# Kernel optimization log

Hardware: AMD Instinct MI355X
Metric: run time of the kernel (lower is better)

## Reference

```python
import jax, jax.numpy as jnp
import numpy as np

DIM_Q = 512
DIM_K = 512
DIM_V = 512
NUM_HEADS = 8
B, NQ, NK = 8, 1024, 1024
EPS = 1e-5


def _layer_norm(x, gamma, beta):
    mu = jnp.mean(x, axis=-1, keepdims=True)
    var = jnp.var(x, axis=-1, keepdims=True)
    return (x - mu) * jax.lax.rsqrt(var + EPS) * gamma + beta


def setup_inputs() -> dict:
    key = jax.random.key(0)
    ks = jax.random.split(key, 12)

    def lin(k, fan_in, fan_out):
        bound = 1.0 / np.sqrt(fan_in)
        kw, kb = jax.random.split(k)
        W = jax.random.uniform(kw, (fan_in, fan_out), jnp.float32, -bound, bound)
        b = jax.random.uniform(kb, (fan_out,), jnp.float32, -bound, bound)
        return W, b

    Q = jax.random.normal(ks[0], (B, NQ, DIM_Q), jnp.float32)
    K = jax.random.normal(ks[1], (B, NK, DIM_K), jnp.float32)
    Wq, bq = lin(ks[2], DIM_Q, DIM_V)
    Wk, bk = lin(ks[3], DIM_K, DIM_V)
    Wv, bv = lin(ks[4], DIM_K, DIM_V)
    Wo, bo = lin(ks[5], DIM_V, DIM_V)
    g0 = jnp.ones((DIM_V,), jnp.float32)
    be0 = jnp.zeros((DIM_V,), jnp.float32)
    g1 = jnp.ones((DIM_V,), jnp.float32)
    be1 = jnp.zeros((DIM_V,), jnp.float32)
    return {"Q": Q, "K": K, "Wq": Wq, "bq": bq, "Wk": Wk, "bk": bk,
            "Wv": Wv, "bv": bv, "Wo": Wo, "bo": bo,
            "g0": g0, "be0": be0, "g1": g1, "be1": be1}


def reference(Q, K, Wq, bq, Wk, bk, Wv, bv, Wo, bo, g0, be0, g1, be1):
    H = NUM_HEADS
    d = DIM_V // H
    b, nq, _ = Q.shape
    nk = K.shape[1]

    Qp = (Q @ Wq + bq).reshape(b, nq, H, d)   # [B,Nq,H,d]
    Kp = (K @ Wk + bk).reshape(b, nk, H, d)   # [B,Nk,H,d]
    Vp = (K @ Wv + bv).reshape(b, nk, H, d)   # [B,Nk,H,d]

    # NOTE: original scales by sqrt(dim_V), not sqrt(head_dim)
    scores = jnp.einsum("bqhd,bkhd->bhqk", Qp, Kp) / jnp.sqrt(
        jnp.asarray(DIM_V, Qp.dtype))
    A = jax.nn.softmax(scores, axis=-1)                     # [B,H,Nq,Nk]
    O = Qp + jnp.einsum("bhqk,bkhd->bqhd", A, Vp)           # residual inside heads
    O = O.reshape(b, nq, DIM_V)
    O = _layer_norm(O, g0, be0)
    O = O + jax.nn.relu(O @ Wo + bo)
    O = _layer_norm(O, g1, be1)
    return O
```

## Files before the change

kernel.cpp:

```cpp
#include <hip/hip_runtime.h>
#include <hip/hip_bf16.h>

typedef __attribute__((ext_vector_type(8))) short short8;
typedef __attribute__((ext_vector_type(4))) short s16x4;
typedef __attribute__((ext_vector_type(4))) float f32x4;

#define DIMV 512
#define NHEAD 8
#define NBATCH 8
#define NQL 1024
#define NKL 1024
#define QSCALE (0.04419417382415922f * 1.44269504088896340f)

__device__ __forceinline__ short f2bf(float f) {
    unsigned int u = __float_as_uint(f);
    unsigned int r = (u + 0x7fffu + ((u >> 16) & 1u)) >> 16;
    return (short)r;
}
__device__ __forceinline__ float bf2f(short s) {
    return __uint_as_float(((unsigned int)(unsigned short)s) << 16);
}
__device__ __forceinline__ unsigned cvt_pk_bf16(float a, float b) {
    unsigned r;
    asm("v_cvt_pk_bf16_f32 %0, %1, %2" : "=v"(r) : "v"(a), "v"(b));
    return r;
}
__device__ __forceinline__ short8 pack8(float4 x, float4 y) {
    union { unsigned u[4]; short8 s; } u;
    u.u[0] = cvt_pk_bf16(x.x, x.y); u.u[1] = cvt_pk_bf16(x.z, x.w);
    u.u[2] = cvt_pk_bf16(y.x, y.y); u.u[3] = cvt_pk_bf16(y.z, y.w);
    return u.s;
}

__global__ void k_transpose_w4(const float* __restrict__ w0, const float* __restrict__ w1,
                               const float* __restrict__ w2, const float* __restrict__ w3,
                               short* __restrict__ t0, short* __restrict__ t1,
                               short* __restrict__ t2, short* __restrict__ t3) {
    __shared__ float tile[32][33];
    const float* W; short* Wt;
    int z = blockIdx.z;
    if (z == 0)      { W = w0; Wt = t0; }
    else if (z == 1) { W = w1; Wt = t1; }
    else if (z == 2) { W = w2; Wt = t2; }
    else             { W = w3; Wt = t3; }
    int tx = threadIdx.x, ty = threadIdx.y;
    int n0 = blockIdx.x * 32, k0 = blockIdx.y * 32;
    #pragma unroll
    for (int r = 0; r < 4; ++r)
        tile[ty + r * 8][tx] = W[(size_t)(k0 + ty + r * 8) * DIMV + n0 + tx];
    __syncthreads();
    #pragma unroll
    for (int r = 0; r < 4; ++r)
        Wt[(size_t)(n0 + ty + r * 8) * DIMV + k0 + tx] = f2bf(tile[tx][ty + r * 8]);
}

__global__ __launch_bounds__(256) void k_transpose_v(const short* __restrict__ KVp,
                                                     short* __restrict__ VT) {
    __shared__ short tile[64][72];
    int tid = threadIdx.x;
    int bid = blockIdx.x;
    int kt = bid & 15, h = (bid >> 4) & 7, b = bid >> 7;
    const short* src = KVp + ((size_t)(b * 1024 + kt * 64)) * 1024 + 512 + h * 64;
    short* dst = VT + ((size_t)(b * 512 + h * 64)) * 1024 + kt * 64;
    #pragma unroll
    for (int p = 0; p < 2; ++p) {
        int idx = p * 256 + tid;
        int r = idx >> 3, dc = (idx & 7) * 8;
        short8 v = *reinterpret_cast<const short8*>(&src[(size_t)r * 1024 + dc]);
        #pragma unroll
        for (int j = 0; j < 8; ++j) tile[dc + j][r] = v[j];
    }
    __syncthreads();
    #pragma unroll
    for (int p = 0; p < 2; ++p) {
        int idx = p * 256 + tid;
        int r = idx >> 3, kc = (idx & 7) * 8;
        *reinterpret_cast<short8*>(&dst[(size_t)r * 1024 + kc]) =
            *reinterpret_cast<const short8*>(&tile[r][kc]);
    }
}

#define GLS 72
template<int MODE, bool AF32, int NBX, int LDC>
__global__ __launch_bounds__(256) void k_gemm(
    const void* __restrict__ Av, const short* __restrict__ Bt,
    const float* __restrict__ bias, const float* __restrict__ bias2,
    short* __restrict__ outB, const short* __restrict__ residB)
{
    __shared__ __align__(16) short As[64 * GLS];
    __shared__ __align__(16) short Bs[64 * GLS];
    int tid = threadIdx.x;
    int lane = tid & 63, wid = tid >> 6;
    int wr = wid >> 1, wc = wid & 1;
    int c = lane & 15, g = lane >> 4;
    int bid = blockIdx.x;
    int xcd = bid & 7, slot = bid >> 3;
    int bx = slot % NBX;
    int by = xcd + 8 * (slot / NBX);
    int m0 = by * 64, n0 = bx * 64;

    int r0 = tid >> 3, kc = (tid & 7) * 8;
    const short* Bg = Bt + (size_t)(n0 + r0) * 512 + kc;

    f32x4 acc[2][2] = {};
    short8 b0 = *reinterpret_cast<const short8*>(Bg);
    short8 b1 = *reinterpret_cast<const short8*>(Bg + 32 * 512);

    if (AF32) {
        const float* Ag = (const float*)Av + (size_t)(m0 + r0) * 512 + kc;
        float4 a00 = *reinterpret_cast<const float4*>(Ag);
        float4 a01 = *reinterpret_cast<const float4*>(Ag + 4);
        float4 a10 = *reinterpret_cast<const float4*>(Ag + 32 * 512);
        float4 a11 = *reinterpret_cast<const float4*>(Ag + 32 * 512 + 4);

        for (int k0 = 0; k0 < 512; k0 += 64) {
            *reinterpret_cast<short8*>(&As[r0 * GLS + kc]) = pack8(a00, a01);
            *reinterpret_cast<short8*>(&As[(r0 + 32) * GLS + kc]) = pack8(a10, a11);
            *reinterpret_cast<short8*>(&Bs[r0 * GLS + kc]) = b0;
            *reinterpret_cast<short8*>(&Bs[(r0 + 32) * GLS + kc]) = b1;
            __syncthreads();
            if (k0 < 448) {
                a00 = *reinterpret_cast<const float4*>(Ag + k0 + 64);
                a01 = *reinterpret_cast<const float4*>(Ag + k0 + 64 + 4);
                a10 = *reinterpret_cast<const float4*>(Ag + k0 + 64 + 32 * 512);
                a11 = *reinterpret_cast<const float4*>(Ag + k0 + 64 + 32 * 512 + 4);
                b0 = *reinterpret_cast<const short8*>(Bg + k0 + 64);
                b1 = *reinterpret_cast<const short8*>(Bg + k0 + 64 + 32 * 512);
            }
            #pragma unroll
            for (int ks = 0; ks < 2; ++ks) {
                short8 af[2], bfr[2];
                #pragma unroll
                for (int i = 0; i < 2; ++i)
                    af[i] = *reinterpret_cast<short8*>(&As[(wr * 32 + i * 16 + c) * GLS + ks * 32 + g * 8]);
                #pragma unroll
                for (int j = 0; j < 2; ++j)
                    bfr[j] = *reinterpret_cast<short8*>(&Bs[(wc * 32 + j * 16 + c) * GLS + ks * 32 + g * 8]);
                #pragma unroll
                for (int i = 0; i < 2; ++i)
                    #pragma unroll
                    for (int j = 0; j < 2; ++j)
                        acc[i][j] = __builtin_amdgcn_mfma_f32_16x16x32_bf16(af[i], bfr[j], acc[i][j], 0, 0, 0);
            }
            __syncthreads();
        }
    } else {
        const short* Ag = (const short*)Av + (size_t)(m0 + r0) * 512 + kc;
        short8 a0 = *reinterpret_cast<const short8*>(Ag);
        short8 a1 = *reinterpret_cast<const short8*>(Ag + 32 * 512);

        for (int k0 = 0; k0 < 512; k0 += 64) {
            *reinterpret_cast<short8*>(&As[r0 * GLS + kc]) = a0;
            *reinterpret_cast<short8*>(&As[(r0 + 32) * GLS + kc]) = a1;
            *reinterpret_cast<short8*>(&Bs[r0 * GLS + kc]) = b0;
            *reinterpret_cast<short8*>(&Bs[(r0 + 32) * GLS + kc]) = b1;
            __syncthreads();
            if (k0 < 448) {
                a0 = *reinterpret_cast<const short8*>(Ag + k0 + 64);
                a1 = *reinterpret_cast<const short8*>(Ag + k0 + 64 + 32 * 512);
                b0 = *reinterpret_cast<const short8*>(Bg + k0 + 64);
                b1 = *reinterpret_cast<const short8*>(Bg + k0 + 64 + 32 * 512);
            }
            #pragma unroll
            for (int ks = 0; ks < 2; ++ks) {
                short8 af[2], bfr[2];
                #pragma unroll
                for (int i = 0; i < 2; ++i)
                    af[i] = *reinterpret_cast<short8*>(&As[(wr * 32 + i * 16 + c) * GLS + ks * 32 + g * 8]);
                #pragma unroll
                for (int j = 0; j < 2; ++j)
                    bfr[j] = *reinterpret_cast<short8*>(&Bs[(wc * 32 + j * 16 + c) * GLS + ks * 32 + g * 8]);
                #pragma unroll
                for (int i = 0; i < 2; ++i)
                    #pragma unroll
                    for (int j = 0; j < 2; ++j)
                        acc[i][j] = __builtin_amdgcn_mfma_f32_16x16x32_bf16(af[i], bfr[j], acc[i][j], 0, 0, 0);
            }
            __syncthreads();
        }
    }

    #pragma unroll
    for (int i = 0; i < 2; ++i)
        #pragma unroll
        for (int j = 0; j < 2; ++j) {
            int row = m0 + wr * 32 + i * 16 + g * 4;
            int col = n0 + wc * 32 + j * 16 + c;
            float bb = (MODE == 1 && n0 >= 512) ? bias2[col - 512] : bias[col];
            #pragma unroll
            for (int q = 0; q < 4; ++q) {
                size_t idx = (size_t)(row + q) * LDC + col;
                float v = acc[i][j][q] + bb;
                if (MODE == 0)      outB[idx] = f2bf(v * QSCALE);
                else if (MODE == 1) outB[idx] = f2bf(v);
                else {
                    size_t ridx = (size_t)(row + q) * 512 + col;
                    outB[idx] = f2bf(bf2f(residB[ridx]) + fmaxf(v, 0.f));
                }
            }
        }
}

__global__ __launch_bounds__(256) void k_attn(
    const short* __restrict__ Qb, const short* __restrict__ Kb,
    const short* __restrict__ VTb, const short* __restrict__ RgBase,
    short* __restrict__ Out)
{
    constexpr float RSCALE = 1.0f / QSCALE;
    __shared__ __align__(16) short Ks[64 * 72];
    __shared__ __align__(16) short Vt[64 * 72];
    __shared__ __align__(16) short Ps[64 * 72];
    int tid = threadIdx.x;
    int lane = tid & 63, w = tid >> 6;
    int c = lane & 15, g = lane >> 4;
    int bid = blockIdx.x;
    int xcd = bid & 7, slot = bid >> 3;
    int qb = slot & 15;
    int grp = xcd + 8 * (slot >> 4);
    int h = grp & 7, b = grp >> 3;
    const short* Qg = Qb + (size_t)(b * NQL + qb * 64) * 512 + h * 64;
    const short* Kg = Kb + (size_t)b * NKL * 1024 + h * 64;
    const short* VTg = VTb + (size_t)(b * 512 + h * 64) * NKL;
    const short* Rg = RgBase + (size_t)(b * NQL + qb * 64) * 512 + h * 64;
    short* Og = Out + (size_t)(b * NQL + qb * 64) * 512 + h * 64;

    short8 qf[2];
    #pragma unroll
    for (int ks = 0; ks < 2; ++ks)
        qf[ks] = *reinterpret_cast<const short8*>(&Qg[(size_t)(w * 16 + c) * 512 + ks * 32 + g * 8]);

    int kr[2], kd[2];
    #pragma unroll
    for (int p = 0; p < 2; ++p) {
        int idx = p * 256 + tid;
        kr[p] = idx >> 3; kd[p] = (idx & 7) * 8;
    }

    short8 kreg[2], vreg[2];
    #pragma unroll
    for (int p = 0; p < 2; ++p) {
        kreg[p] = *reinterpret_cast<const short8*>(&Kg[(size_t)kr[p] * 1024 + kd[p]]);
        vreg[p] = *reinterpret_cast<const short8*>(&VTg[(size_t)kr[p] * 1024 + kd[p]]);
    }
    #pragma unroll
    for (int p = 0; p < 2; ++p) {
        *reinterpret_cast<short8*>(&Ks[kr[p] * 72 + kd[p]]) = kreg[p];
        *reinterpret_cast<short8*>(&Vt[kr[p] * 72 + kd[p]]) = vreg[p];
    }
    __syncthreads();

    float m = -1e30f, l = 0.f;
    f32x4 o[4] = {};

    for (int t = 0; t < 16; ++t) {
        if (t < 15) {
            const short* Kn = Kg + (size_t)(t + 1) * 64 * 1024;
            const short* Vn = VTg + (size_t)(t + 1) * 64;
            #pragma unroll
            for (int p = 0; p < 2; ++p) {
                kreg[p] = *reinterpret_cast<const short8*>(&Kn[(size_t)kr[p] * 1024 + kd[p]]);
                vreg[p] = *reinterpret_cast<const short8*>(&Vn[(size_t)kr[p] * 1024 + kd[p]]);
            }
        }

        f32x4 s[4] = {};
        #pragma unroll
        for (int ks = 0; ks < 2; ++ks) {
            #pragma unroll
            for (int i = 0; i < 4; ++i) {
                short8 ak = *reinterpret_cast<short8*>(&Ks[(i * 16 + c) * 72 + ks * 32 + g * 8]);
                s[i] = __builtin_amdgcn_mfma_f32_16x16x32_bf16(ak, qf[ks], s[i], 0, 0, 0);
            }
        }

        float r0 = fmaxf(fmaxf(s[0][0], s[0][1]), fmaxf(s[0][2], s[0][3]));
        float r1 = fmaxf(fmaxf(s[1][0], s[1][1]), fmaxf(s[1][2], s[1][3]));
        float r2 = fmaxf(fmaxf(s[2][0], s[2][1]), fmaxf(s[2][2], s[2][3]));
        float r3 = fmaxf(fmaxf(s[3][0], s[3][1]), fmaxf(s[3][2], s[3][3]));
        float rowm = fmaxf(fmaxf(r0, r1), fmaxf(r2, r3));
        rowm = fmaxf(rowm, __shfl_xor(rowm, 16));
        rowm = fmaxf(rowm, __shfl_xor(rowm, 32));
        if (!__all(rowm <= m + 8.f)) {
            float mnew = fmaxf(m, rowm);
            float corr = __builtin_amdgcn_exp2f(m - mnew);
            l *= corr;
            float cq[4];
            #pragma unroll
            for (int q = 0; q < 4; ++q) cq[q] = __shfl(corr, g * 4 + q);
            #pragma unroll
            for (int jf = 0; jf < 4; ++jf)
                #pragma unroll
                for (int q = 0; q < 4; ++q)
                    o[jf][q] *= cq[q];
            m = mnew;
        }
        float psum = 0.f;
        #pragma unroll
        for (int i = 0; i < 4; ++i) {
            float p0 = __builtin_amdgcn_exp2f(s[i][0] - m);
            float p1 = __builtin_amdgcn_exp2f(s[i][1] - m);
            float p2 = __builtin_amdgcn_exp2f(s[i][2] - m);
            float p3 = __builtin_amdgcn_exp2f(s[i][3] - m);
            psum += (p0 + p1) + (p2 + p3);
            uint2 pw;
            pw.x = cvt_pk_bf16(p0, p1);
            pw.y = cvt_pk_bf16(p2, p3);
            *reinterpret_cast<uint2*>(&Ps[(w * 16 + c) * 72 + i * 16 + g * 4]) = pw;
        }
        psum += __shfl_xor(psum, 16);
        psum += __shfl_xor(psum, 32);
        l += psum;

        #pragma unroll
        for (int ks = 0; ks < 2; ++ks) {
            short8 pa = *reinterpret_cast<short8*>(&Ps[(w * 16 + c) * 72 + ks * 32 + g * 8]);
            #pragma unroll
            for (int jf = 0; jf < 4; ++jf) {
                short8 vb = *reinterpret_cast<short8*>(&Vt[(jf * 16 + c) * 72 + ks * 32 + g * 8]);
                o[jf] = __builtin_amdgcn_mfma_f32_16x16x32_bf16(pa, vb, o[jf], 0, 0, 0);
            }
        }

        if (t < 15) {
            __syncthreads();
            #pragma unroll
            for (int p = 0; p < 2; ++p) {
                *reinterpret_cast<short8*>(&Ks[kr[p] * 72 + kd[p]]) = kreg[p];
                *reinterpret_cast<short8*>(&Vt[kr[p] * 72 + kd[p]]) = vreg[p];
            }
            __syncthreads();
        }
    }

    float linv = 1.f / l;
    float lq[4];
    #pragma unroll
    for (int q = 0; q < 4; ++q) lq[q] = __shfl(linv, g * 4 + q);
    #pragma unroll
    for (int jf = 0; jf < 4; ++jf)
        #pragma unroll
        for (int q = 0; q < 4; ++q) {
            int r = w * 16 + g * 4 + q;
            int d = jf * 16 + c;
            size_t idx = (size_t)r * 512 + d;
            Og[idx] = f2bf(o[jf][q] * lq[q] + bf2f(Rg[idx]) * RSCALE);
        }
}

__global__ __launch_bounds__(64) void k_ln(
    const short* __restrict__ inB,
    float* __restrict__ outF, short* __restrict__ outB,
    const float* __restrict__ gamma, const float* __restrict__ beta)
{
    int row = blockIdx.x, lane = threadIdx.x;
    float vals[8];
    short8 v = *reinterpret_cast<const short8*>(&inB[(size_t)row * 512 + lane * 8]);
    #pragma unroll
    for (int j = 0; j < 8; ++j) vals[j] = bf2f(v[j]);
    float sum = 0.f, sq = 0.f;
    #pragma unroll
    for (int j = 0; j < 8; ++j) { sum += vals[j]; sq += vals[j] * vals[j]; }
    #pragma unroll
    for (int mask = 32; mask; mask >>= 1) {
        sum += __shfl_xor(sum, mask);
        sq  += __shfl_xor(sq, mask);
    }
    float mean = sum * (1.f / 512.f);
    float var  = sq * (1.f / 512.f) - mean * mean;
    float rstd = rsqrtf(var + 1e-5f);
    float y[8];
    #pragma unroll
    for (int j = 0; j < 8; ++j) {
        int col = lane * 8 + j;
        y[j] = (vals[j] - mean) * rstd * gamma[col] + beta[col];
    }
    size_t base = (size_t)row * 512 + lane * 8;
    if (outF) {
        float4 o0 = {y[0], y[1], y[2], y[3]};
        float4 o1 = {y[4], y[5], y[6], y[7]};
        *reinterpret_cast<float4*>(&outF[base]) = o0;
        *reinterpret_cast<float4*>(&outF[base + 4]) = o1;
    }
    if (outB) {
        int4 p;
        p.x = cvt_pk_bf16(y[0], y[1]); p.y = cvt_pk_bf16(y[2], y[3]);
        p.z = cvt_pk_bf16(y[4], y[5]); p.w = cvt_pk_bf16(y[6], y[7]);
        *reinterpret_cast<int4*>(&outB[base]) = p;
    }
}

extern "C" void kernel_launch(void* const* d_in, const int* in_sizes, int n_in,
                              void* d_out, int out_size, void* d_ws, size_t ws_size,
                              hipStream_t stream) {
    const float* Q   = (const float*)d_in[0];
    const float* K   = (const float*)d_in[1];
    const float* Wq  = (const float*)d_in[2];
    const float* bq  = (const float*)d_in[3];
    const float* Wk  = (const float*)d_in[4];
    const float* bk  = (const float*)d_in[5];
    const float* Wv  = (const float*)d_in[6];
    const float* bv  = (const float*)d_in[7];
    const float* Wo  = (const float*)d_in[8];
    const float* bo  = (const float*)d_in[9];
    const float* g0  = (const float*)d_in[10];
    const float* be0 = (const float*)d_in[11];
    const float* g1  = (const float*)d_in[12];
    const float* be1 = (const float*)d_in[13];
    float* out = (float*)d_out;
    char* ws = (char*)d_ws;
    const size_t MB = 1024 * 1024;

    short* Oa    = (short*)(ws + 0);
    short* Wqt   = (short*)(ws + 16 * MB);
    short* Wkvt  = (short*)(ws + 16 * MB + 512 * 1024);
    short* Wot   = (short*)(ws + 17 * MB + 512 * 1024);
    short* VT    = (short*)(ws + 18 * MB);
    short* Qpb   = (short*)(ws + 34 * MB);
    short* KVp   = (short*)(ws + 42 * MB);
    short* ln0b  = (short*)(ws + 34 * MB);
    short* out2b = (short*)(ws + 42 * MB);

    dim3 tb(32, 8), tg(16, 16, 4);
    k_transpose_w4<<<tg, tb, 0, stream>>>(Wq, Wk, Wv, Wo,
                                          Wqt, Wkvt, Wkvt + 512 * 512, Wot);

    k_gemm<0, true, 8, 512><<<1024, 256, 0, stream>>>(Q, Wqt, bq, nullptr, Qpb, nullptr);
    k_gemm<1, true, 16, 1024><<<2048, 256, 0, stream>>>(K, Wkvt, bk, bv, KVp, nullptr);

    k_transpose_v<<<NBATCH * NHEAD * 16, 256, 0, stream>>>(KVp, VT);

    k_attn<<<NBATCH * NHEAD * (NQL / 64), 256, 0, stream>>>(Qpb, KVp, VT, Qpb, Oa);

    k_ln<<<NBATCH * NQL, 64, 0, stream>>>(Oa, nullptr, ln0b, g0, be0);
    k_gemm<2, false, 8, 512><<<1024, 256, 0, stream>>>(ln0b, Wot, bo, nullptr, out2b, ln0b);
    k_ln<<<NBATCH * NQL, 64, 0, stream>>>(out2b, out, nullptr, g1, be1);
}
```

Measured before the change: 110.1 us.

## Double-buffer attention K/V tiles via direct global-to-LDS loads with swizzle

The attention kernel now stages K and V^T tiles with global_load_lds straight into double-buffered, XOR-swizzled shared memory, replacing register staging and two barriers per iteration with one. Blocks grow to 512 threads covering 128 query rows, so each K/V tile is reused by twice as many waves. The aim is to overlap tile loads with MFMA work, cut LDS bank conflicts and halve K/V traffic per query. In exchange, LDS use per block rises, fewer blocks run (512), the XCD-aware block mapping is dropped, and the code relies on the async LDS load finishing before the single barrier.

```diff
diff --git a/kernel.cpp b/kernel.cpp
--- a/kernel.cpp
+++ b/kernel.cpp
@@ -30,6 +30,11 @@
     u.u[0] = cvt_pk_bf16(x.x, x.y); u.u[1] = cvt_pk_bf16(x.z, x.w);
     u.u[2] = cvt_pk_bf16(y.x, y.y); u.u[3] = cvt_pk_bf16(y.z, y.w);
     return u.s;
+}
+__device__ __forceinline__ void gload16(const void* g, void* l) {
+    __builtin_amdgcn_global_load_lds(
+        (const __attribute__((address_space(1))) unsigned int*)g,
+        (__attribute__((address_space(3))) unsigned int*)l, 16, 0, 0);
 }
 
 __global__ void k_transpose_w4(const float* __restrict__ w0, const float* __restrict__ w1,
@@ -201,66 +206,54 @@
         }
 }
 
-__global__ __launch_bounds__(256) void k_attn(
+__global__ __launch_bounds__(512) void k_attn(
     const short* __restrict__ Qb, const short* __restrict__ Kb,
     const short* __restrict__ VTb, const short* __restrict__ RgBase,
     short* __restrict__ Out)
 {
     constexpr float RSCALE = 1.0f / QSCALE;
-    __shared__ __align__(16) short Ks[64 * 72];
-    __shared__ __align__(16) short Vt[64 * 72];
-    __shared__ __align__(16) short Ps[64 * 72];
+    __shared__ __align__(16) short Ks[2][64 * 64];
+    __shared__ __align__(16) short Vt[2][64 * 64];
+    __shared__ __align__(16) short Ps[128 * 72];
     int tid = threadIdx.x;
     int lane = tid & 63, w = tid >> 6;
     int c = lane & 15, g = lane >> 4;
     int bid = blockIdx.x;
-    int xcd = bid & 7, slot = bid >> 3;
-    int qb = slot & 15;
-    int grp = xcd + 8 * (slot >> 4);
+    int grp = bid & 63, qb = bid >> 6;
     int h = grp & 7, b = grp >> 3;
-    const short* Qg = Qb + (size_t)(b * NQL + qb * 64) * 512 + h * 64;
+    const short* Qg = Qb + (size_t)(b * NQL + qb * 128) * 512 + h * 64;
     const short* Kg = Kb + (size_t)b * NKL * 1024 + h * 64;
     const short* VTg = VTb + (size_t)(b * 512 + h * 64) * NKL;
-    const short* Rg = RgBase + (size_t)(b * NQL + qb * 64) * 512 + h * 64;
-    short* Og = Out + (size_t)(b * NQL + qb * 64) * 512 + h * 64;
+    const short* Rg = RgBase + (size_t)(b * NQL + qb * 128) * 512 + h * 64;
+    short* Og = Out + (size_t)(b * NQL + qb * 128) * 512 + h * 64;
 
     short8 qf[2];
     #pragma unroll
     for (int ks = 0; ks < 2; ++ks)
         qf[ks] = *reinterpret_cast<const short8*>(&Qg[(size_t)(w * 16 + c) * 512 + ks * 32 + g * 8]);
 
-    int kr[2], kd[2];
-    #pragma unroll
-    for (int p = 0; p < 2; ++p) {
-        int idx = p * 256 + tid;
-        kr[p] = idx >> 3; kd[p] = (idx & 7) * 8;
-    }
-
-    short8 kreg[2], vreg[2];
-    #pragma unroll
-    for (int p = 0; p < 2; ++p) {
-        kreg[p] = *reinterpret_cast<const short8*>(&Kg[(size_t)kr[p] * 1024 + kd[p]]);
-        vreg[p] = *reinterpret_cast<const short8*>(&VTg[(size_t)kr[p] * 1024 + kd[p]]);
-    }
-    #pragma unroll
-    for (int p = 0; p < 2; ++p) {
-        *reinterpret_cast<short8*>(&Ks[kr[p] * 72 + kd[p]]) = kreg[p];
-        *reinterpret_cast<short8*>(&Vt[kr[p] * 72 + kd[p]]) = vreg[p];
-    }
+    int sr = tid >> 3, ss = tid & 7;
+    int sg = ss ^ (sr & 7);
+    const short* Kgc = Kg + (size_t)sr * 1024 + sg * 8;
+    const short* Vgc = VTg + (size_t)sr * 1024 + sg * 8;
+    char* KsB = (char*)&Ks[0][0];
+    char* VtB = (char*)&Vt[0][0];
+    int wbase = (tid & ~63) * 16;
+
+    gload16(Kgc, KsB + wbase);
+    gload16(Vgc, VtB + wbase);
     __syncthreads();
 
     float m = -1e30f, l = 0.f;
     f32x4 o[4] = {};
+    int swz = (c & 7) * 8;
 
     for (int t = 0; t < 16; ++t) {
+        int cur = t & 1;
         if (t < 15) {
-            const short* Kn = Kg + (size_t)(t + 1) * 64 * 1024;
-            const short* Vn = VTg + (size_t)(t + 1) * 64;
-            #pragma unroll
-            for (int p = 0; p < 2; ++p) {
-                kreg[p] = *reinterpret_cast<const short8*>(&Kn[(size_t)kr[p] * 1024 + kd[p]]);
-                vreg[p] = *reinterpret_cast<const short8*>(&Vn[(size_t)kr[p] * 1024 + kd[p]]);
-            }
+            int nxt = cur ^ 1;
+            gload16(Kgc + (size_t)(t + 1) * 64 * 1024, KsB + nxt * 8192 + wbase);
+            gload16(Vgc + (t + 1) * 64, VtB + nxt * 8192 + wbase);
         }
 
         f32x4 s[4] = {};
@@ -268,7 +261,8 @@
         for (int ks = 0; ks < 2; ++ks) {
             #pragma unroll
             for (int i = 0; i < 4; ++i) {
-                short8 ak = *reinterpret_cast<short8*>(&Ks[(i * 16 + c) * 72 + ks * 32 + g * 8]);
+                short8 ak = *reinterpret_cast<short8*>(
+                    &Ks[cur][(i * 16 + c) * 64 + (((ks * 4 + g) * 8) ^ swz)]);
                 s[i] = __builtin_amdgcn_mfma_f32_16x16x32_bf16(ak, qf[ks], s[i], 0, 0, 0);
             }
         }
@@ -316,20 +310,13 @@
             short8 pa = *reinterpret_cast<short8*>(&Ps[(w * 16 + c) * 72 + ks * 32 + g * 8]);
             #pragma unroll
             for (int jf = 0; jf < 4; ++jf) {
-                short8 vb = *reinterpret_cast<short8*>(&Vt[(jf * 16 + c) * 72 + ks * 32 + g * 8]);
+                short8 vb = *reinterpret_cast<short8*>(
+                    &Vt[cur][(jf * 16 + c) * 64 + (((ks * 4 + g) * 8) ^ swz)]);
                 o[jf] = __builtin_amdgcn_mfma_f32_16x16x32_bf16(pa, vb, o[jf], 0, 0, 0);
             }
         }
 
-        if (t < 15) {
-            __syncthreads();
-            #pragma unroll
-            for (int p = 0; p < 2; ++p) {
-                *reinterpret_cast<short8*>(&Ks[kr[p] * 72 + kd[p]]) = kreg[p];
-                *reinterpret_cast<short8*>(&Vt[kr[p] * 72 + kd[p]]) = vreg[p];
-            }
-            __syncthreads();
-        }
+        __syncthreads();
     }
 
     float linv = 1.f / l;
@@ -429,7 +416,7 @@
 
     k_transpose_v<<<NBATCH * NHEAD * 16, 256, 0, stream>>>(KVp, VT);
 
-    k_attn<<<NBATCH * NHEAD * (NQL / 64), 256, 0, stream>>>(Qpb, KVp, VT, Qpb, Oa);
+    k_attn<<<NBATCH * NHEAD * (NQL / 128), 512, 0, stream>>>(Qpb, KVp, VT, Qpb, Oa);
 
     k_ln<<<NBATCH * NQL, 64, 0, stream>>>(Oa, nullptr, ln0b, g0, be0);
     k_gemm<2, false, 8, 512><<<1024, 256, 0, stream>>>(ln0b, Wot, bo, nullptr, out2b, ln0b);
```

Result: faster. 101.6 us (-7.7%).
